# Optimization experiments

Hardware: AMD Instinct MI355X
Metric: run time of the kernel (lower is better)

The kernel has to match this reference:

```python
import jax, jax.numpy as jnp
import numpy as np

N, IN_DIM, HID, OUT_DIM = 200000, 64, 128, 64
E = 3200000


def setup_inputs() -> dict:
    key = jax.random.key(0)
    ks = jax.random.split(key, 24)
    s_in = 1.0 / np.sqrt(IN_DIM)
    s_h = 1.0 / np.sqrt(HID)
    inp = {
        "x": jax.random.normal(ks[0], (N, IN_DIM), jnp.float32),
        "edge_index": jax.random.randint(ks[1], (2, E), 0, N, jnp.int64),
        "batch": jnp.zeros((N,), jnp.int64),
        # input projections W_{i,f,c,o}: [IN_DIM, HID]
        "W_i": jax.random.normal(ks[2], (IN_DIM, HID), jnp.float32) * s_in,
        "W_f": jax.random.normal(ks[3], (IN_DIM, HID), jnp.float32) * s_in,
        "W_c": jax.random.normal(ks[4], (IN_DIM, HID), jnp.float32) * s_in,
        "W_o": jax.random.normal(ks[5], (IN_DIM, HID), jnp.float32) * s_in,
        # ChebConv(K=1) weights on H: Theta0 [HID, HID] + conv bias [HID]
        "Wg_i": jax.random.normal(ks[6], (HID, HID), jnp.float32) * s_h,
        "Wg_f": jax.random.normal(ks[7], (HID, HID), jnp.float32) * s_h,
        "Wg_c": jax.random.normal(ks[8], (HID, HID), jnp.float32) * s_h,
        "Wg_o": jax.random.normal(ks[9], (HID, HID), jnp.float32) * s_h,
        "bg_i": jax.random.normal(ks[10], (HID,), jnp.float32) * 0.02,
        "bg_f": jax.random.normal(ks[11], (HID,), jnp.float32) * 0.02,
        "bg_c": jax.random.normal(ks[12], (HID,), jnp.float32) * 0.02,
        "bg_o": jax.random.normal(ks[13], (HID,), jnp.float32) * 0.02,
        # peephole weights w_c_* [1, HID] and gate biases b_* [1, HID]
        "wc_i": jax.random.normal(ks[14], (1, HID), jnp.float32) * 0.02,
        "wc_f": jax.random.normal(ks[15], (1, HID), jnp.float32) * 0.02,
        "wc_o": jax.random.normal(ks[16], (1, HID), jnp.float32) * 0.02,
        "b_i": jax.random.normal(ks[17], (1, HID), jnp.float32) * 0.02,
        "b_f": jax.random.normal(ks[18], (1, HID), jnp.float32) * 0.02,
        "b_c": jax.random.normal(ks[19], (1, HID), jnp.float32) * 0.02,
        "b_o": jax.random.normal(ks[20], (1, HID), jnp.float32) * 0.02,
        # final fc: [HID, OUT_DIM]
        "fc_W": jax.random.normal(ks[21], (HID, OUT_DIM), jnp.float32) * s_h,
        "fc_b": jax.random.normal(ks[22], (OUT_DIM,), jnp.float32) * 0.02,
    }
    return inp


def _gclstm_step(x, H, C, W_i, W_f, W_c, W_o, Wg_i, Wg_f, Wg_c, Wg_o,
                 bg_i, bg_f, bg_c, bg_o, wc_i, wc_f, wc_o, b_i, b_f, b_c, b_o):
    # ChebConv with K=1: T_0(L) = I, so conv(H) = H @ Theta0 + bias (edge_index is a no-op)
    conv = lambda Wg, bg: H @ Wg + bg
    i = jax.nn.sigmoid(x @ W_i + conv(Wg_i, bg_i) + wc_i * C + b_i)
    f = jax.nn.sigmoid(x @ W_f + conv(Wg_f, bg_f) + wc_f * C + b_f)
    t = jnp.tanh(x @ W_c + conv(Wg_c, bg_c) + b_c)
    C_new = f * C + i * t
    o = jax.nn.sigmoid(x @ W_o + conv(Wg_o, bg_o) + wc_o * C_new + b_o)
    H_new = o * jnp.tanh(C_new)
    return H_new, C_new


def reference(x, edge_index, batch, W_i, W_f, W_c, W_o, Wg_i, Wg_f, Wg_c, Wg_o,
              bg_i, bg_f, bg_c, bg_o, wc_i, wc_f, wc_o, b_i, b_f, b_c, b_o,
              fc_W, fc_b):
    # H=None, C=None in the original call -> zeros init, single LSTM step
    H0 = jnp.zeros((x.shape[0], W_i.shape[1]), x.dtype)
    C0 = jnp.zeros_like(H0)
    H, C = _gclstm_step(x, H0, C0, W_i, W_f, W_c, W_o, Wg_i, Wg_f, Wg_c, Wg_o,
                        bg_i, bg_f, bg_c, bg_o, wc_i, wc_f, wc_o,
                        b_i, b_f, b_c, b_o)
    return H @ fc_W + fc_b  # [N, OUT_DIM]
```

## Files before the change

kernel.cpp:

```cpp
#include <hip/hip_runtime.h>


typedef __attribute__((ext_vector_type(8))) short short8;
typedef __attribute__((ext_vector_type(4))) float f32x4;
typedef __attribute__((ext_vector_type(4))) unsigned uint4_t;

#define N_ROWS 200000
#define IN_DIM 64
#define HID 128
#define OUT_DIM 64

#define WFRAG_ELEMS (24 * 2 * 64 * 8)
#define FCFRAG_OFF  49152
#define FCFRAG_ELEMS (4 * 4 * 64 * 8)
#define BIAS_OFF    65536
#define BIAS_FLOATS 576

__device__ __forceinline__ short f2bf(float f) {
  unsigned u = __float_as_uint(f);
  u += 0x7FFFu + ((u >> 16) & 1u);
  return (short)(u >> 16);
}
__device__ __forceinline__ unsigned cvt_pk_bf16(float lo, float hi) {
  unsigned r;
  asm("v_cvt_pk_bf16_f32 %0, %1, %2" : "=v"(r) : "v"(lo), "v"(hi));
  return r;
}
__device__ __forceinline__ float fexp2(float z) { return __builtin_amdgcn_exp2f(z); }
__device__ __forceinline__ float frcp(float z)  { return __builtin_amdgcn_rcpf(z); }
__device__ __forceinline__ float fsigmoid(float z) {
  return frcp(1.0f + fexp2(-1.44269504f * z));
}
__device__ __forceinline__ float ftanh(float z) {
  return 1.0f - 2.0f * frcp(1.0f + fexp2(2.88539008f * z));
}
__device__ __forceinline__ int hperm(int g, int d) {
  return 32 * (g >> 1) + 2 * (g & 1) + 8 * (d >> 2) + 4 * ((d >> 1) & 1) + (d & 1);
}

__global__ void repack_kernel(const float* __restrict__ W_i, const float* __restrict__ W_c,
                              const float* __restrict__ W_o, const float* __restrict__ fc_W,
                              const float* __restrict__ bg_i, const float* __restrict__ bg_c,
                              const float* __restrict__ bg_o,
                              const float* __restrict__ b_i, const float* __restrict__ b_c,
                              const float* __restrict__ b_o, const float* __restrict__ wc_o,
                              const float* __restrict__ fc_b,
                              short* __restrict__ wfrag, short* __restrict__ fcfrag,
                              float* __restrict__ bias) {
  int tid = blockIdx.x * blockDim.x + threadIdx.x;
  const int total1 = WFRAG_ELEMS;
  const int total2 = FCFRAG_ELEMS;
  for (int e = tid; e < total1 + total2 + HID + OUT_DIM; e += gridDim.x * blockDim.x) {
    if (e < total1) {
      int j = e & 7, lane = (e >> 3) & 63, s = (e >> 9) & 1, t = e >> 10;
      int q = lane >> 4, cidx = lane & 15;
      int gate = t >> 3;
      int g = t & 7;
      int h = hperm(g, cidx);
      int feat = 32 * s + 8 * q + j;
      const float* W = (gate == 0) ? W_i : ((gate == 1) ? W_c : W_o);
      wfrag[e] = f2bf(W[feat * HID + h]);
    } else if (e < total1 + total2) {
      int e2 = e - total1;
      int j = e2 & 7, lane = (e2 >> 3) & 63, s = (e2 >> 9) & 3, t = e2 >> 11;
      int q = lane >> 4, cidx = lane & 15;
      int od = 16 * t + cidx;
      int hid = 32 * s + 8 * q + j;
      fcfrag[e2] = f2bf(fc_W[hid * OUT_DIM + od]);
    } else if (e < total1 + total2 + HID) {
      int p = e - total1 - total2;
      int h = hperm(p >> 4, p & 15);
      bias[p]           = bg_i[h] + b_i[h];
      bias[HID + p]     = bg_c[h] + b_c[h];
      bias[2 * HID + p] = bg_o[h] + b_o[h];
      bias[3 * HID + p] = wc_o[h];
    } else {
      int h2 = e - total1 - total2 - HID;
      bias[4 * HID + h2] = fc_b[h2];
    }
  }
}

__global__ __launch_bounds__(512, 4) void gclstm_fused(
    const float* __restrict__ x, const short* __restrict__ wfrag,
    const short* __restrict__ fcfrag, const float* __restrict__ bias,
    float* __restrict__ out) {
  __shared__ __align__(16) char smem[49152 + BIAS_FLOATS * 4];
  short* Wl = (short*)smem;
  float* Bl = (float*)(smem + 49152);

  const int tid = threadIdx.x;
  {
    const uint4_t* src = (const uint4_t*)wfrag;
    uint4_t* dst = (uint4_t*)Wl;
#pragma unroll
    for (int k = 0; k < 6; ++k) dst[k * 512 + tid] = src[k * 512 + tid];
    if (tid < BIAS_FLOATS / 4)
      ((uint4_t*)Bl)[tid] = ((const uint4_t*)bias)[tid];
  }
  __syncthreads();

  const int lane = tid & 63;
  const int wslot = tid >> 6;
  const int wid = blockIdx.x * 8 + wslot;
  const int row0 = wid * 32;
  if (row0 >= N_ROWS) return;
  const int q = lane >> 4, c = lane & 15;
  const short* wfl = Wl + lane * 8;
  const short* ff  = fcfrag + lane * 8;

  short8 bx[2][2];
  union U { unsigned u[4]; short8 s8; };
#pragma unroll
  for (int m = 0; m < 2; ++m) {
    const float* xr = x + (size_t)(row0 + 16 * m + c) * IN_DIM + 8 * q;
#pragma unroll
    for (int sk = 0; sk < 2; ++sk) {
      f32x4 f0 = *(const f32x4*)(xr + 32 * sk);
      f32x4 f1 = *(const f32x4*)(xr + 32 * sk + 4);
      U v;
      v.u[0] = cvt_pk_bf16(f0[0], f0[1]);
      v.u[1] = cvt_pk_bf16(f0[2], f0[3]);
      v.u[2] = cvt_pk_bf16(f1[0], f1[1]);
      v.u[3] = cvt_pk_bf16(f1[2], f1[3]);
      bx[m][sk] = v.s8;
    }
  }

  const float* Bi  = Bl;
  const float* Bc  = Bl + HID;
  const float* Bo  = Bl + 2 * HID;
  const float* Wco = Bl + 3 * HID;
  const float* Fcb = Bl + 4 * HID;

  unsigned hbuf[8][2][2];
#pragma unroll
  for (int g = 0; g < 8; ++g) {
    const int p0 = g * 16 + 4 * q;
    f32x4 vbi = *(const f32x4*)(Bi + p0);
    f32x4 vbc = *(const f32x4*)(Bc + p0);
    f32x4 vbo = *(const f32x4*)(Bo + p0);
    f32x4 vwc = *(const f32x4*)(Wco + p0);
    f32x4 acc[3][2];
#pragma unroll
    for (int m = 0; m < 2; ++m) { acc[0][m] = vbi; acc[1][m] = vbc; acc[2][m] = vbo; }
#pragma unroll
    for (int sk = 0; sk < 2; ++sk) {
      short8 ai = *(const short8*)(wfl + ((g     ) * 2 + sk) * 512);
      short8 ac = *(const short8*)(wfl + ((g +  8) * 2 + sk) * 512);
      short8 ao = *(const short8*)(wfl + ((g + 16) * 2 + sk) * 512);
#pragma unroll
      for (int m = 0; m < 2; ++m) {
        acc[0][m] = __builtin_amdgcn_mfma_f32_16x16x32_bf16(ai, bx[m][sk], acc[0][m], 0, 0, 0);
        acc[1][m] = __builtin_amdgcn_mfma_f32_16x16x32_bf16(ac, bx[m][sk], acc[1][m], 0, 0, 0);
        acc[2][m] = __builtin_amdgcn_mfma_f32_16x16x32_bf16(ao, bx[m][sk], acc[2][m], 0, 0, 0);
      }
    }
#pragma unroll
    for (int m = 0; m < 2; ++m) {
      float hw[4];
#pragma unroll
      for (int r = 0; r < 4; ++r) {
        float gi = fsigmoid(acc[0][m][r]);
        float gt = ftanh(acc[1][m][r]);
        float C  = gi * gt;
        float go = fsigmoid(acc[2][m][r] + vwc[r] * C);
        hw[r] = go * ftanh(C);
      }
      hbuf[g][m][0] = cvt_pk_bf16(hw[0], hw[1]);
      hbuf[g][m][1] = cvt_pk_bf16(hw[2], hw[3]);
    }
  }

  f32x4 oacc[4][2];
#pragma unroll
  for (int t = 0; t < 4; ++t) {
    f32x4 fb = *(const f32x4*)(Fcb + 16 * t + 4 * q);
    oacc[t][0] = fb; oacc[t][1] = fb;
  }
#pragma unroll
  for (int s = 0; s < 4; ++s) {
#pragma unroll
    for (int m = 0; m < 2; ++m) {
      U bu;
      bu.u[0] = hbuf[2 * s][m][0];
      bu.u[1] = hbuf[2 * s + 1][m][0];
      bu.u[2] = hbuf[2 * s][m][1];
      bu.u[3] = hbuf[2 * s + 1][m][1];
#pragma unroll
      for (int t = 0; t < 4; ++t) {
        short8 af = *(const short8*)(ff + (t * 4 + s) * 512);
        oacc[t][m] = __builtin_amdgcn_mfma_f32_16x16x32_bf16(af, bu.s8, oacc[t][m], 0, 0, 0);
      }
    }
  }

#pragma unroll
  for (int t = 0; t < 4; ++t) {
    const int od0 = 16 * t + 4 * q;
#pragma unroll
    for (int m = 0; m < 2; ++m) {
      *(f32x4*)(out + (size_t)(row0 + 16 * m + c) * OUT_DIM + od0) = oacc[t][m];
    }
  }
}

extern "C" void kernel_launch(void* const* d_in, const int* in_sizes, int n_in,
                              void* d_out, int out_size, void* d_ws, size_t ws_size,
                              hipStream_t stream) {
  (void)in_sizes; (void)n_in; (void)out_size; (void)ws_size;
  const float* x    = (const float*)d_in[0];
  const float* W_i  = (const float*)d_in[3];
  const float* W_c  = (const float*)d_in[5];
  const float* W_o  = (const float*)d_in[6];
  const float* bg_i = (const float*)d_in[11];
  const float* bg_c = (const float*)d_in[13];
  const float* bg_o = (const float*)d_in[14];
  const float* wc_o = (const float*)d_in[17];
  const float* b_i  = (const float*)d_in[18];
  const float* b_c  = (const float*)d_in[20];
  const float* b_o  = (const float*)d_in[21];
  const float* fc_W = (const float*)d_in[22];
  const float* fc_b = (const float*)d_in[23];

  short* wfrag  = (short*)d_ws;
  short* fcfrag = (short*)((char*)d_ws + FCFRAG_OFF);
  float* bias   = (float*)((char*)d_ws + BIAS_OFF);

  repack_kernel<<<dim3(64), dim3(256), 0, stream>>>(
      W_i, W_c, W_o, fc_W, bg_i, bg_c, bg_o, b_i, b_c, b_o, wc_o, fc_b,
      wfrag, fcfrag, bias);

  const int nwaves = N_ROWS / 32;
  const int nwg = (nwaves + 7) / 8;
  gclstm_fused<<<dim3(nwg), dim3(512), 0, stream>>>(
      x, wfrag, fcfrag, bias, (float*)d_out);
}
```

Measured before the change: 50.17 us.

## Fold activation scales into weights, merge reciprocals, drop LDS weight staging

```diff
diff --git a/kernel.cpp b/kernel.cpp
--- a/kernel.cpp
+++ b/kernel.cpp
@@ -3,18 +3,19 @@
 
 typedef __attribute__((ext_vector_type(8))) short short8;
 typedef __attribute__((ext_vector_type(4))) float f32x4;
-typedef __attribute__((ext_vector_type(4))) unsigned uint4_t;
 
 #define N_ROWS 200000
 #define IN_DIM 64
 #define HID 128
 #define OUT_DIM 64
 
+#define LOG2E 1.44269504f
+#define TWOLOG2E 2.88539008f
+
 #define WFRAG_ELEMS (24 * 2 * 64 * 8)
 #define FCFRAG_OFF  49152
 #define FCFRAG_ELEMS (4 * 4 * 64 * 8)
 #define BIAS_OFF    65536
-#define BIAS_FLOATS 576
 
 __device__ __forceinline__ short f2bf(float f) {
   unsigned u = __float_as_uint(f);
@@ -28,12 +29,6 @@
 }
 __device__ __forceinline__ float fexp2(float z) { return __builtin_amdgcn_exp2f(z); }
 __device__ __forceinline__ float frcp(float z)  { return __builtin_amdgcn_rcpf(z); }
-__device__ __forceinline__ float fsigmoid(float z) {
-  return frcp(1.0f + fexp2(-1.44269504f * z));
-}
-__device__ __forceinline__ float ftanh(float z) {
-  return 1.0f - 2.0f * frcp(1.0f + fexp2(2.88539008f * z));
-}
 __device__ __forceinline__ int hperm(int g, int d) {
   return 32 * (g >> 1) + 2 * (g & 1) + 8 * (d >> 2) + 4 * ((d >> 1) & 1) + (d & 1);
 }
@@ -59,7 +54,8 @@
       int h = hperm(g, cidx);
       int feat = 32 * s + 8 * q + j;
       const float* W = (gate == 0) ? W_i : ((gate == 1) ? W_c : W_o);
-      wfrag[e] = f2bf(W[feat * HID + h]);
+      float scale = (gate == 1) ? TWOLOG2E : -LOG2E;
+      wfrag[e] = f2bf(W[feat * HID + h] * scale);
     } else if (e < total1 + total2) {
       int e2 = e - total1;
       int j = e2 & 7, lane = (e2 >> 3) & 63, s = (e2 >> 9) & 3, t = e2 >> 11;
@@ -70,10 +66,10 @@
     } else if (e < total1 + total2 + HID) {
       int p = e - total1 - total2;
       int h = hperm(p >> 4, p & 15);
-      bias[p]           = bg_i[h] + b_i[h];
-      bias[HID + p]     = bg_c[h] + b_c[h];
-      bias[2 * HID + p] = bg_o[h] + b_o[h];
-      bias[3 * HID + p] = wc_o[h];
+      bias[p]           = -LOG2E  * (bg_i[h] + b_i[h]);
+      bias[HID + p]     = TWOLOG2E * (bg_c[h] + b_c[h]);
+      bias[2 * HID + p] = -LOG2E  * (bg_o[h] + b_o[h]);
+      bias[3 * HID + p] = -LOG2E  * wc_o[h];
     } else {
       int h2 = e - total1 - total2 - HID;
       bias[4 * HID + h2] = fc_b[h2];
@@ -81,39 +77,23 @@
   }
 }
 
-__global__ __launch_bounds__(512, 4) void gclstm_fused(
+__global__ __launch_bounds__(64, 4) void gclstm_fused(
     const float* __restrict__ x, const short* __restrict__ wfrag,
     const short* __restrict__ fcfrag, const float* __restrict__ bias,
     float* __restrict__ out) {
-  __shared__ __align__(16) char smem[49152 + BIAS_FLOATS * 4];
-  short* Wl = (short*)smem;
-  float* Bl = (float*)(smem + 49152);
-
-  const int tid = threadIdx.x;
-  {
-    const uint4_t* src = (const uint4_t*)wfrag;
-    uint4_t* dst = (uint4_t*)Wl;
-#pragma unroll
-    for (int k = 0; k < 6; ++k) dst[k * 512 + tid] = src[k * 512 + tid];
-    if (tid < BIAS_FLOATS / 4)
-      ((uint4_t*)Bl)[tid] = ((const uint4_t*)bias)[tid];
-  }
-  __syncthreads();
-
-  const int lane = tid & 63;
-  const int wslot = tid >> 6;
-  const int wid = blockIdx.x * 8 + wslot;
-  const int row0 = wid * 32;
-  if (row0 >= N_ROWS) return;
+  const int lane = threadIdx.x;
+  const int wid = blockIdx.x;
+  const size_t row0 = (size_t)wid * 32;
   const int q = lane >> 4, c = lane & 15;
-  const short* wfl = Wl + lane * 8;
-  const short* ff  = fcfrag + lane * 8;
+  const short* wf = wfrag + lane * 8;
+  const short* ff = fcfrag + lane * 8;
+
+  union U { unsigned u[4]; short8 s8; };
 
   short8 bx[2][2];
-  union U { unsigned u[4]; short8 s8; };
 #pragma unroll
   for (int m = 0; m < 2; ++m) {
-    const float* xr = x + (size_t)(row0 + 16 * m + c) * IN_DIM + 8 * q;
+    const float* xr = x + (row0 + 16 * m + c) * IN_DIM + 8 * q;
 #pragma unroll
     for (int sk = 0; sk < 2; ++sk) {
       f32x4 f0 = *(const f32x4*)(xr + 32 * sk);
@@ -127,28 +107,28 @@
     }
   }
 
-  const float* Bi  = Bl;
-  const float* Bc  = Bl + HID;
-  const float* Bo  = Bl + 2 * HID;
-  const float* Wco = Bl + 3 * HID;
-  const float* Fcb = Bl + 4 * HID;
+  const float* Si  = bias;
+  const float* Sc  = bias + HID;
+  const float* So  = bias + 2 * HID;
+  const float* Swc = bias + 3 * HID;
+  const float* Fcb = bias + 4 * HID;
 
   unsigned hbuf[8][2][2];
 #pragma unroll
   for (int g = 0; g < 8; ++g) {
     const int p0 = g * 16 + 4 * q;
-    f32x4 vbi = *(const f32x4*)(Bi + p0);
-    f32x4 vbc = *(const f32x4*)(Bc + p0);
-    f32x4 vbo = *(const f32x4*)(Bo + p0);
-    f32x4 vwc = *(const f32x4*)(Wco + p0);
+    f32x4 vbi = *(const f32x4*)(Si + p0);
+    f32x4 vbc = *(const f32x4*)(Sc + p0);
+    f32x4 vbo = *(const f32x4*)(So + p0);
+    f32x4 vwc = *(const f32x4*)(Swc + p0);
     f32x4 acc[3][2];
 #pragma unroll
     for (int m = 0; m < 2; ++m) { acc[0][m] = vbi; acc[1][m] = vbc; acc[2][m] = vbo; }
 #pragma unroll
     for (int sk = 0; sk < 2; ++sk) {
-      short8 ai = *(const short8*)(wfl + ((g     ) * 2 + sk) * 512);
-      short8 ac = *(const short8*)(wfl + ((g +  8) * 2 + sk) * 512);
-      short8 ao = *(const short8*)(wfl + ((g + 16) * 2 + sk) * 512);
+      short8 ai = *(const short8*)(wf + ((g     ) * 2 + sk) * 512);
+      short8 ac = *(const short8*)(wf + ((g +  8) * 2 + sk) * 512);
+      short8 ao = *(const short8*)(wf + ((g + 16) * 2 + sk) * 512);
 #pragma unroll
       for (int m = 0; m < 2; ++m) {
         acc[0][m] = __builtin_amdgcn_mfma_f32_16x16x32_bf16(ai, bx[m][sk], acc[0][m], 0, 0, 0);
@@ -158,17 +138,26 @@
     }
 #pragma unroll
     for (int m = 0; m < 2; ++m) {
-      float hw[4];
-#pragma unroll
-      for (int r = 0; r < 4; ++r) {
-        float gi = fsigmoid(acc[0][m][r]);
-        float gt = ftanh(acc[1][m][r]);
-        float C  = gi * gt;
-        float go = fsigmoid(acc[2][m][r] + vwc[r] * C);
-        hw[r] = go * ftanh(C);
-      }
-      hbuf[g][m][0] = cvt_pk_bf16(hw[0], hw[1]);
-      hbuf[g][m][1] = cvt_pk_bf16(hw[2], hw[3]);
+      f32x4 ei, ec;
+#pragma unroll
+      for (int r = 0; r < 4; ++r) { ei[r] = fexp2(acc[0][m][r]); ec[r] = fexp2(acc[1][m][r]); }
+      f32x4 den1 = (ei + 1.0f) * (ec + 1.0f);
+      f32x4 rd1;
+#pragma unroll
+      for (int r = 0; r < 4; ++r) rd1[r] = frcp(den1[r]);
+      f32x4 C = (ec - 1.0f) * rd1;
+      f32x4 s2 = acc[2][m] + vwc * C;
+      f32x4 t2 = C * TWOLOG2E;
+      f32x4 eo, e2;
+#pragma unroll
+      for (int r = 0; r < 4; ++r) { eo[r] = fexp2(s2[r]); e2[r] = fexp2(t2[r]); }
+      f32x4 den2 = (eo + 1.0f) * (e2 + 1.0f);
+      f32x4 rd2;
+#pragma unroll
+      for (int r = 0; r < 4; ++r) rd2[r] = frcp(den2[r]);
+      f32x4 H = (e2 - 1.0f) * rd2;
+      hbuf[g][m][0] = cvt_pk_bf16(H[0], H[1]);
+      hbuf[g][m][1] = cvt_pk_bf16(H[2], H[3]);
     }
   }
 
@@ -200,7 +189,7 @@
     const int od0 = 16 * t + 4 * q;
 #pragma unroll
     for (int m = 0; m < 2; ++m) {
-      *(f32x4*)(out + (size_t)(row0 + 16 * m + c) * OUT_DIM + od0) = oacc[t][m];
+      *(f32x4*)(out + (row0 + 16 * m + c) * OUT_DIM + od0) = oacc[t][m];
     }
   }
 }
@@ -231,8 +220,7 @@
       W_i, W_c, W_o, fc_W, bg_i, bg_c, bg_o, b_i, b_c, b_o, wc_o, fc_b,
       wfrag, fcfrag, bias);
 
-  const int nwaves = N_ROWS / 32;
-  const int nwg = (nwaves + 7) / 8;
-  gclstm_fused<<<dim3(nwg), dim3(512), 0, stream>>>(
+  const int nwg = N_ROWS / 32;
+  gclstm_fused<<<dim3(nwg), dim3(64), 0, stream>>>(
       x, wfrag, fcfrag, bias, (float*)d_out);
 }
```

Result: no change. 49.54 us (-1.3%).
